# Performance work log

Hardware: AMD Instinct MI355X
Metric: run time of the kernel (lower is better)

## Reference

```python
import jax, jax.numpy as jnp
import numpy as np

N_NODES = 50000
N_EDGES = 800000
N_FEAT = 128
HID = 256
N_GRAPHS = 512


def _glorot(key, shape):
    fan_in, fan_out = shape[0], shape[1]
    s = jnp.sqrt(6.0 / (fan_in + fan_out))
    return jax.random.uniform(key, shape, jnp.float32, -s, s)


def setup_inputs() -> dict:
    key = jax.random.key(0)
    ks = jax.random.split(key, 10)
    x = jax.random.normal(ks[0], (N_NODES, N_FEAT), jnp.float32)
    edge_index = jax.random.randint(ks[1], (2, N_EDGES), 0, N_NODES, jnp.int64)
    batch = jnp.sort(jax.random.randint(ks[2], (N_NODES,), 0, N_GRAPHS, jnp.int64))
    y = jax.random.randint(ks[3], (N_GRAPHS,), 0, 2, jnp.int32)
    params = {
        "W1": _glorot(ks[4], (N_FEAT, HID)), "b1": jnp.zeros((HID,), jnp.float32),
        "W2": _glorot(ks[5], (HID, HID // 2)), "b2": jnp.zeros((HID // 2,), jnp.float32),
        "W3": _glorot(ks[6], (HID // 2, HID // 4)), "b3": jnp.zeros((HID // 4,), jnp.float32),
        "Wl": _glorot(ks[7], (HID // 4, 1)), "bl": jnp.zeros((1,), jnp.float32),
    }
    return {"x": x, "edge_index": edge_index, "batch": batch, "y": y, **params}


def gcn_conv(x, src, dst, dinv, W, b):
    # PyG GCNConv: x' = D^{-1/2}(A+I)D^{-1/2} x W + b, with self-loops.
    h = x @ W  # [N, out]
    norm = dinv[src] * dinv[dst]  # [E]
    agg = jax.ops.segment_sum(h[src] * norm[:, None], dst, num_segments=x.shape[0])
    agg = agg + h * (dinv * dinv)[:, None]  # self-loop contribution
    return agg + b


def reference(x, edge_index, batch, y, W1, b1, W2, b2, W3, b3, Wl, bl):
    n = x.shape[0]
    src, dst = edge_index[0], edge_index[1]
    # degree of A + I (in-degree on dst, plus self-loop)
    deg = jax.ops.segment_sum(jnp.ones_like(dst, dtype=x.dtype), dst, num_segments=n) + 1.0
    dinv = jax.lax.rsqrt(deg)

    h = jax.nn.relu(gcn_conv(x, src, dst, dinv, W1, b1))
    h = jax.nn.relu(gcn_conv(h, src, dst, dinv, W2, b2))
    h = gcn_conv(h, src, dst, dinv, W3, b3)

    # global mean pool over graphs
    sums = jax.ops.segment_sum(h, batch, num_segments=N_GRAPHS)
    counts = jax.ops.segment_sum(jnp.ones((n,), h.dtype), batch, num_segments=N_GRAPHS)
    pooled = sums / jnp.maximum(counts, 1.0)[:, None]

    logits = pooled @ Wl + bl  # [G, 1]
    t = y.reshape(-1, 1).astype(logits.dtype)
    # BCEWithLogitsLoss (mean, numerically stable)
    loss = jnp.mean(jnp.maximum(logits, 0.0) - logits * t + jnp.log1p(jnp.exp(-jnp.abs(logits))))
    out = jax.nn.sigmoid(logits)
    return (out, loss)
```

## Files before the change

kernel.cpp:

```cpp
#include <hip/hip_runtime.h>
#include <hip/hip_bf16.h>

typedef short s8v __attribute__((ext_vector_type(8)));
typedef float f4v __attribute__((ext_vector_type(4)));
typedef float f2v __attribute__((ext_vector_type(2)));
typedef unsigned short u16;
typedef unsigned char u8;

#define EPB 16384
#define NBKT 196

__device__ __forceinline__ float bf2f(short u) {
    unsigned int x = ((unsigned int)(unsigned short)u) << 16;
    return __builtin_bit_cast(float, x);
}
__device__ __forceinline__ short f2bf(float f) {
    unsigned int u = __builtin_bit_cast(unsigned int, f);
    unsigned int r = (u + 0x7FFF + ((u >> 16) & 1)) >> 16;
    return (short)r;
}
__device__ __forceinline__ short h16(float f) {
    return (short)(__builtin_bit_cast(unsigned int, f) >> 16);
}
__device__ __forceinline__ void dec16_add(uint4 u, float* acc) {
    f2v p;
    p = __builtin_amdgcn_cvt_pk_f32_fp8(u.x, false); acc[0] += p[0];  acc[1] += p[1];
    p = __builtin_amdgcn_cvt_pk_f32_fp8(u.x, true);  acc[2] += p[0];  acc[3] += p[1];
    p = __builtin_amdgcn_cvt_pk_f32_fp8(u.y, false); acc[4] += p[0];  acc[5] += p[1];
    p = __builtin_amdgcn_cvt_pk_f32_fp8(u.y, true);  acc[6] += p[0];  acc[7] += p[1];
    p = __builtin_amdgcn_cvt_pk_f32_fp8(u.z, false); acc[8] += p[0];  acc[9] += p[1];
    p = __builtin_amdgcn_cvt_pk_f32_fp8(u.z, true);  acc[10] += p[0]; acc[11] += p[1];
    p = __builtin_amdgcn_cvt_pk_f32_fp8(u.w, false); acc[12] += p[0]; acc[13] += p[1];
    p = __builtin_amdgcn_cvt_pk_f32_fp8(u.w, true);  acc[14] += p[0]; acc[15] += p[1];
}
__device__ __forceinline__ s8v dec8_bf16(unsigned lo, unsigned hi) {
    f2v p0 = __builtin_amdgcn_cvt_pk_f32_fp8(lo, false);
    f2v p1 = __builtin_amdgcn_cvt_pk_f32_fp8(lo, true);
    f2v p2 = __builtin_amdgcn_cvt_pk_f32_fp8(hi, false);
    f2v p3 = __builtin_amdgcn_cvt_pk_f32_fp8(hi, true);
    s8v r;
    r[0] = h16(p0[0]); r[1] = h16(p0[1]); r[2] = h16(p1[0]); r[3] = h16(p1[1]);
    r[4] = h16(p2[0]); r[5] = h16(p2[1]); r[6] = h16(p3[0]); r[7] = h16(p3[1]);
    return r;
}
template<bool HI>
__device__ __forceinline__ unsigned pk2(float a, float b, unsigned old) {
    return __builtin_amdgcn_cvt_pk_fp8_f32(a, b, old, HI);
}
__device__ __forceinline__ u8 enc1(float v) {
    return (u8)(__builtin_amdgcn_cvt_pk_fp8_f32(v, v, 0, false) & 0xff);
}

__global__ __launch_bounds__(256)
void k_fat(const int* __restrict__ dst, int e, int* __restrict__ hist_t, int nbA,
           const float* __restrict__ W1, const float* __restrict__ W2,
           const float* __restrict__ W3, const float* __restrict__ Wl,
           const float* __restrict__ b3, short* __restrict__ Bt1,
           short* __restrict__ Bt2, const int* __restrict__ batch, int n, int ngr,
           int* __restrict__ gstart, u8* __restrict__ xs8,
           float* __restrict__ w3l, float* __restrict__ wb) {
    int blk = blockIdx.x, tid = threadIdx.x;
    if (blk < nbA) {
        __shared__ int h[NBKT];
        if (tid < NBKT) h[tid] = 0;
        __syncthreads();
        int base = blk * EPB;
        int end = min(base + EPB, e);
        for (int i = base + tid * 4; i < end; i += 1024) {
            if (i + 3 < end) {
                int4 d = *(const int4*)(dst + i);
                atomicAdd(&h[d.x >> 8], 1);
                atomicAdd(&h[d.y >> 8], 1);
                atomicAdd(&h[d.z >> 8], 1);
                atomicAdd(&h[d.w >> 8], 1);
            } else {
                for (int k = i; k < end; ++k) atomicAdd(&h[dst[k] >> 8], 1);
            }
        }
        __syncthreads();
        if (tid < NBKT) hist_t[tid * nbA + blk] = h[tid];
    } else if (blk < nbA + 256) {
        int id = (blk - nbA) * 256 + tid;
        if (id < 32768) {
            int c = id >> 7, k = id & 127;
            Bt1[id] = f2bf(W1[k * 256 + c]);
        } else {
            int i = id - 32768;
            int c = i >> 8, k = i & 255;
            Bt2[i] = f2bf(W2[k * 128 + c]);
        }
    } else if (blk < nbA + 259) {
        int g = (blk - nbA - 256) * 256 + tid;
        if (g > ngr) return;
        if (g == ngr) { gstart[g] = n; return; }
        int lo = 0, hi = n;
        while (lo < hi) { int mid = (lo + hi) >> 1; if (batch[mid] < g) lo = mid + 1; else hi = mid; }
        gstart[g] = lo;
    } else if (blk == nbA + 259) {
        if (tid < 32) ((unsigned*)xs8)[(size_t)n * 32 + tid] = 0;
    } else {
        if (tid < 128) {
            float s = 0.f;
            #pragma unroll 4
            for (int c = 0; c < 64; ++c) s = fmaf(W3[tid * 64 + c], Wl[c], s);
            w3l[tid] = s;
        } else if (tid == 128) {
            float s = 0.f;
            for (int c = 0; c < 64; ++c) s = fmaf(b3[c], Wl[c], s);
            wb[0] = s;
        }
    }
}

__global__ __launch_bounds__(1024)
void k_scanall(int* __restrict__ a, int nelem) {
    __shared__ int ws[16];
    int tid = threadIdx.x, lane = tid & 63, w = tid >> 6;
    int base = tid * 10;
    int v[10];
    int s = 0;
    #pragma unroll
    for (int k = 0; k < 10; ++k) { v[k] = (base + k < nelem) ? a[base + k] : 0; s += v[k]; }
    int x = s;
    #pragma unroll
    for (int d = 1; d < 64; d <<= 1) {
        int t2 = __shfl_up(x, d, 64);
        if (lane >= d) x += t2;
    }
    if (lane == 63) ws[w] = x;
    __syncthreads();
    if (w == 0 && lane < 16) {
        int vv = ws[lane];
        int xx = vv;
        #pragma unroll
        for (int d = 1; d < 16; d <<= 1) {
            int t2 = __shfl_up(xx, d, 64);
            if (lane >= d) xx += t2;
        }
        ws[lane] = xx - vv;
    }
    __syncthreads();
    int run = ws[w] + (x - s);
    #pragma unroll
    for (int k = 0; k < 10; ++k) {
        if (base + k < nelem) a[base + k] = run;
        run += v[k];
    }
}

__global__ __launch_bounds__(256)
void k_part(const int* __restrict__ src, const int* __restrict__ dst, int e,
            const int* __restrict__ offs, int nbA, unsigned* __restrict__ parted) {
    __shared__ int cur[NBKT];
    int tid = threadIdx.x, blk = blockIdx.x;
    if (tid < NBKT) cur[tid] = offs[tid * nbA + blk];
    __syncthreads();
    int base = blk * EPB;
    int end = min(base + EPB, e);
    for (int i = base + tid * 4; i < end; i += 1024) {
        if (i + 3 < end) {
            int4 d = *(const int4*)(dst + i);
            int4 s = *(const int4*)(src + i);
            int p;
            p = atomicAdd(&cur[d.x >> 8], 1); parted[p] = (unsigned)s.x | ((unsigned)(d.x & 255) << 16);
            p = atomicAdd(&cur[d.y >> 8], 1); parted[p] = (unsigned)s.y | ((unsigned)(d.y & 255) << 16);
            p = atomicAdd(&cur[d.z >> 8], 1); parted[p] = (unsigned)s.z | ((unsigned)(d.z & 255) << 16);
            p = atomicAdd(&cur[d.w >> 8], 1); parted[p] = (unsigned)s.w | ((unsigned)(d.w & 255) << 16);
        } else {
            for (int k = i; k < end; ++k) {
                int d = dst[k];
                int p = atomicAdd(&cur[d >> 8], 1);
                parted[p] = (unsigned)src[k] | ((unsigned)(d & 255) << 16);
            }
        }
    }
}

__global__ __launch_bounds__(256)
void k_lists(const unsigned* __restrict__ parted, const int* __restrict__ offs,
             int nbA, int e, const float* __restrict__ x, u16* __restrict__ csrcp,
             int* __restrict__ deg, float* __restrict__ dinv,
             u8* __restrict__ xs8, int n) {
    __shared__ u16 lists[256 * 64];
    __shared__ int cnt[256];
    int tid = threadIdx.x, bkt = blockIdx.x;
    for (int k = tid; k < 16384; k += 256) lists[k] = 0xFFFF;
    cnt[tid] = 0;
    __syncthreads();
    int base = offs[bkt * nbA];
    int end = (bkt == NBKT - 1) ? e : offs[(bkt + 1) * nbA];
    for (int i = base + tid; i < end; i += 256) {
        unsigned p = parted[i];
        int dl = (int)((p >> 16) & 0xFF);
        int r = atomicAdd(&cnt[dl], 1);
        if (r < 64) lists[dl * 64 + r] = (u16)(p & 0xFFFF);
    }
    __syncthreads();
    const s8v* lsrc = (const s8v*)lists;
    s8v* ldst = (s8v*)(csrcp + (size_t)bkt * (256 * 64));
    for (int k = tid; k < 2048; k += 256) ldst[k] = lsrc[k];
    int node = bkt * 256 + tid;
    deg[node] = min(cnt[tid], 64);
    dinv[node] = rsqrtf((float)cnt[tid] + 1.0f);
    #pragma unroll 1
    for (int r16 = 0; r16 < 16; ++r16) {
        int local = r16 * 16 + (tid >> 4);
        int row = bkt * 256 + local;
        if (row >= n) continue;
        float dv = rsqrtf((float)cnt[local] + 1.0f);
        int cg = (tid & 15) * 8;
        f4v a = *(const f4v*)(x + (size_t)row * 128 + cg);
        f4v b = *(const f4v*)(x + (size_t)row * 128 + cg + 4);
        unsigned w0 = pk2<false>(a[0] * dv, a[1] * dv, 0);
        w0 = pk2<true>(a[2] * dv, a[3] * dv, w0);
        unsigned w1 = pk2<false>(b[0] * dv, b[1] * dv, 0);
        w1 = pk2<true>(b[2] * dv, b[3] * dv, w1);
        uint2 o = {w0, w1};
        *(uint2*)(xs8 + (size_t)row * 128 + cg) = o;
    }
}

template<int K, int NT, int CT, bool BIAS, bool RELU, bool DVS, bool ZROW>
__global__ __launch_bounds__(256)
void k_gemm(const u8* __restrict__ A8, const short* __restrict__ Bt,
            const float* __restrict__ bias, const float* __restrict__ dinv,
            u8* __restrict__ C8, int M) {
    constexpr int S = K / 32;
    constexpr int N = NT * 16 * CT;
    if (ZROW && blockIdx.x == 0 && threadIdx.x < N) {
        C8[(size_t)M * N + threadIdx.x] = 0;
    }
    const int lane = threadIdx.x & 63;
    const int gw = (blockIdx.x * 256 + threadIdx.x) >> 6;
    const int nw = (gridDim.x * 256) >> 6;
    const int colset = gw % CT;
    const int strip0 = gw / CT;
    const int sstr = nw / CT;
    const int l15 = lane & 15, l4 = lane >> 4;
    const int colbase = colset * (NT * 16);

    s8v bfr[NT][S];
    float bcol[NT];
    #pragma unroll
    for (int nt = 0; nt < NT; ++nt) {
        int col = colbase + nt * 16 + l15;
        if (BIAS) bcol[nt] = bias[col];
        const short* bp = Bt + (size_t)col * K + l4 * 8;
        #pragma unroll
        for (int s = 0; s < S; ++s)
            bfr[nt][s] = *(const s8v*)(bp + s * 32);
    }

    const int nstrips = M >> 4;
    int strip = strip0;
    if (strip >= nstrips) return;
    uint2 cur[S];
    {
        const u8* arow = A8 + (size_t)(strip * 16 + l15) * K + l4 * 8;
        #pragma unroll
        for (int s = 0; s < S; ++s) cur[s] = *(const uint2*)(arow + s * 32);
    }
    while (true) {
        int nstrip = strip + sstr;
        bool has = nstrip < nstrips;
        uint2 nxt[S];
        if (has) {
            const u8* arow = A8 + (size_t)(nstrip * 16 + l15) * K + l4 * 8;
            #pragma unroll
            for (int s = 0; s < S; ++s) nxt[s] = *(const uint2*)(arow + s * 32);
        }
        f4v acc[NT];
        #pragma unroll
        for (int nt = 0; nt < NT; ++nt) acc[nt] = (f4v){0.f, 0.f, 0.f, 0.f};
        #pragma unroll
        for (int s = 0; s < S; ++s) {
            s8v av = dec8_bf16(cur[s].x, cur[s].y);
            #pragma unroll
            for (int nt = 0; nt < NT; ++nt)
                acc[nt] = __builtin_amdgcn_mfma_f32_16x16x32_bf16(av, bfr[nt][s], acc[nt], 0, 0, 0);
        }
        int orow = strip * 16 + l4 * 4;
        f4v dvr;
        if (DVS) dvr = *(const f4v*)(dinv + orow);
        #pragma unroll
        for (int nt = 0; nt < NT; ++nt) {
            int col = colbase + nt * 16 + l15;
            #pragma unroll
            for (int r = 0; r < 4; ++r) {
                float v = acc[nt][r];
                if (DVS) v *= dvr[r];
                if (BIAS) v += bcol[nt];
                if (RELU) v = fmaxf(v, 0.f);
                C8[(size_t)(orow + r) * N + col] = enc1(v);
            }
        }
        if (!has) break;
        strip = nstrip;
        #pragma unroll
        for (int s = 0; s < S; ++s) cur[s] = nxt[s];
    }
}

template<bool RELU, bool BIAS, bool STORE, bool QPROJ>
__global__ __launch_bounds__(256, 2)
void k_agg(const u8* __restrict__ h8, const u16* __restrict__ csrcp,
           const int* __restrict__ deg, const float* __restrict__ bias,
           u8* __restrict__ outp, int n,
           const float* __restrict__ w3l, float* __restrict__ q) {
    int node = (blockIdx.x * 256 + threadIdx.x) >> 3;
    if (node >= n) return;
    int t = threadIdx.x & 7;
    int c0 = t * 16;
    const u8* hp = h8 + c0;
    float acc[16];
    #pragma unroll
    for (int j = 0; j < 16; ++j) acc[j] = 0.f;
    dec16_add(*(const uint4*)(hp + (size_t)node * 128), acc);

    int dg = deg[node];
    int nch = (dg + 7) >> 3;
    const u16* ep = csrcp + (size_t)node * 64;
    for (int c = 0; c < nch; ++c) {
        int idx = (int)ep[c * 8 + t];
        uint4 buf[8];
        #pragma unroll
        for (int j = 0; j < 8; ++j) {
            unsigned s = (unsigned)__shfl(idx, j, 8);
            s = s < (unsigned)n ? s : (unsigned)n;
            buf[j] = *(const uint4*)(hp + (size_t)s * 128);
        }
        #pragma unroll
        for (int j = 0; j < 8; ++j) dec16_add(buf[j], acc);
    }

    float dv = rsqrtf((float)dg + 1.0f);
    float out[16];
    #pragma unroll
    for (int j = 0; j < 16; ++j) {
        float b = BIAS ? bias[c0 + j] : 0.f;
        out[j] = dv * acc[j] + b;
        if (RELU) out[j] = fmaxf(out[j], 0.f);
    }
    if (STORE) {
        uint4 o;
        o.x = pk2<false>(out[0], out[1], 0);   o.x = pk2<true>(out[2], out[3], o.x);
        o.y = pk2<false>(out[4], out[5], 0);   o.y = pk2<true>(out[6], out[7], o.y);
        o.z = pk2<false>(out[8], out[9], 0);   o.z = pk2<true>(out[10], out[11], o.z);
        o.w = pk2<false>(out[12], out[13], 0); o.w = pk2<true>(out[14], out[15], o.w);
        *(uint4*)(outp + (size_t)node * 128 + c0) = o;
    }
    if (QPROJ) {
        float part = 0.f;
        #pragma unroll
        for (int j = 0; j < 16; ++j) part = fmaf(out[j], w3l[c0 + j], part);
        #pragma unroll
        for (int d = 4; d > 0; d >>= 1) part += __shfl_down(part, d, 8);
        if (t == 0) q[node] = dv * part;
    }
}

__global__ __launch_bounds__(256)
void k_gpool(const float* __restrict__ q, const u16* __restrict__ csrcp,
             const int* __restrict__ deg, const int* __restrict__ gstart,
             const float* __restrict__ wb, const float* __restrict__ bl,
             const int* __restrict__ y, float* __restrict__ out,
             float* __restrict__ plos) {
    __shared__ float red[256];
    int g = blockIdx.x;
    int s = gstart[g], e = gstart[g + 1];
    float local = 0.f;
    float b3l = wb[0];
    for (int v = s + threadIdx.x; v < e; v += 256) {
        int dg = deg[v];
        float acc = q[v];
        const u16* ep = csrcp + (size_t)v * 64;
        for (int c = 0; c < dg; ++c)
            acc += q[ep[c]];
        local += rsqrtf((float)dg + 1.f) * acc + b3l;
    }
    red[threadIdx.x] = local;
    __syncthreads();
    for (int st = 128; st > 0; st >>= 1) {
        if (threadIdx.x < st) red[threadIdx.x] += red[threadIdx.x + st];
        __syncthreads();
    }
    if (threadIdx.x == 0) {
        float cnt = fmaxf((float)(e - s), 1.f);
        float l = red[0] / cnt + bl[0];
        out[g] = 1.f / (1.f + expf(-l));
        float t = (float)y[g];
        plos[g] = fmaxf(l, 0.f) - l * t + log1pf(expf(-fabsf(l)));
    }
}

__global__ void k_loss(const float* __restrict__ plos, float* __restrict__ out) {
    __shared__ float red[512];
    int g = threadIdx.x;
    red[g] = plos[g];
    __syncthreads();
    for (int s = 256; s > 0; s >>= 1) {
        if (g < s) red[g] += red[g + s];
        __syncthreads();
    }
    if (g == 0) out[512] = red[0] / 512.f;
}

extern "C" void kernel_launch(void* const* d_in, const int* in_sizes, int n_in,
                              void* d_out, int out_size, void* d_ws, size_t ws_size,
                              hipStream_t stream) {
    const float* x   = (const float*)d_in[0];
    const int* ei    = (const int*)d_in[1];
    const int* batch = (const int*)d_in[2];
    const int* y     = (const int*)d_in[3];
    const float* W1  = (const float*)d_in[4];
    const float* b1  = (const float*)d_in[5];
    const float* W2  = (const float*)d_in[6];
    const float* b2  = (const float*)d_in[7];
    const float* W3  = (const float*)d_in[8];
    const float* b3  = (const float*)d_in[9];
    const float* Wl  = (const float*)d_in[10];
    const float* bl  = (const float*)d_in[11];

    const int n = in_sizes[2];
    const int e = in_sizes[1] / 2;
    const int ngr = 512;
    const int nbA = (e + EPB - 1) / EPB;
    const int TE = NBKT * nbA;
    const int nrows = NBKT * 256;

    char* ws = (char*)d_ws;
    size_t off = 0;
    auto alloc = [&](size_t bytes) {
        char* p = ws + off;
        off = (off + bytes + 255) & ~(size_t)255;
        return p;
    };
    int*      offs   = (int*)alloc((size_t)TE * 4);
    unsigned* parted = (unsigned*)alloc((size_t)e * 4);
    u16*      csrcp  = (u16*)alloc((size_t)nrows * 64 * 2);
    int*      deg    = (int*)alloc((size_t)nrows * 4);
    float*    dinv   = (float*)alloc((size_t)nrows * 4);
    u8*       xs8    = (u8*)alloc((size_t)(n + 1) * 128);
    u8*       t18    = (u8*)alloc((size_t)n * 128);
    u8*       h18    = (u8*)alloc((size_t)n * 256);
    u8*       g28    = (u8*)alloc((size_t)(n + 1) * 128);
    float*    q      = (float*)alloc((size_t)n * 4);
    int*      gstart = (int*)alloc((size_t)(ngr + 1) * 4);
    short*    Bt1    = (short*)alloc((size_t)32768 * 2);
    short*    Bt2    = (short*)alloc((size_t)32768 * 2);
    float*    w3l    = (float*)alloc((size_t)128 * 4);
    float*    wb     = (float*)alloc((size_t)4 * 4);
    float*    plos   = (float*)alloc((size_t)ngr * 4);

    k_fat<<<nbA + 261, 256, 0, stream>>>(ei + e, e, offs, nbA, W1, W2, W3, Wl, b3,
                                         Bt1, Bt2, batch, n, ngr, gstart, xs8,
                                         w3l, wb);
    k_scanall<<<1, 1024, 0, stream>>>(offs, TE);
    k_part<<<nbA, 256, 0, stream>>>(ei, ei + e, e, offs, nbA, parted);
    k_lists<<<NBKT, 256, 0, stream>>>(parted, offs, nbA, e, x, csrcp, deg, dinv, xs8, n);

    const int gagg = (n * 8 + 255) / 256;
    k_agg<false, false, true, false><<<gagg, 256, 0, stream>>>(
        xs8, csrcp, deg, nullptr, t18, n, nullptr, nullptr);
    k_gemm<128, 4, 4, true, true, false, false><<<256, 256, 0, stream>>>(
        t18, Bt1, b1, nullptr, h18, n);
    k_gemm<256, 2, 4, false, false, true, true><<<256, 256, 0, stream>>>(
        h18, Bt2, nullptr, dinv, g28, n);
    k_agg<true, true, false, true><<<gagg, 256, 0, stream>>>(
        g28, csrcp, deg, b2, nullptr, n, w3l, q);
    k_gpool<<<ngr, 256, 0, stream>>>(q, csrcp, deg, gstart, wb, bl, y,
                                     (float*)d_out, plos);
    k_loss<<<1, 512, 0, stream>>>(plos, (float*)d_out);
}
```

Before: 133.0 us.

## Halve edge partition block size, remap GEMM warps, parallelize pooling, fuse loss reduction

Halves edges per partition block, which doubles the histogram/partition block count, and widens the scan to 20 elements per thread to cover the larger table. The GEMM now has each block own one row strip and assigns its four waves to the four column sets, instead of spreading strips across global waves. Graph pooling uses four lanes per node to walk the neighbor list. The separate loss kernel is removed in favor of an atomicAdd into a slot zeroed in the first kernel. Together these aim to cut launch count, add parallelism to pooling, and improve A-tile sharing in the GEMM. The cost is float atomics, which make the loss sum order nondeterministic.

```diff
diff --git a/kernel.cpp b/kernel.cpp
--- a/kernel.cpp
+++ b/kernel.cpp
@@ -7,7 +7,7 @@
 typedef unsigned short u16;
 typedef unsigned char u8;
 
-#define EPB 16384
+#define EPB 8192
 #define NBKT 196
 
 __device__ __forceinline__ float bf2f(short u) {
@@ -58,7 +58,8 @@
            const float* __restrict__ b3, short* __restrict__ Bt1,
            short* __restrict__ Bt2, const int* __restrict__ batch, int n, int ngr,
            int* __restrict__ gstart, u8* __restrict__ xs8,
-           float* __restrict__ w3l, float* __restrict__ wb) {
+           float* __restrict__ w3l, float* __restrict__ wb,
+           float* __restrict__ outp) {
     int blk = blockIdx.x, tid = threadIdx.x;
     if (blk < nbA) {
         __shared__ int h[NBKT];
@@ -108,6 +109,8 @@
             float s = 0.f;
             for (int c = 0; c < 64; ++c) s = fmaf(b3[c], Wl[c], s);
             wb[0] = s;
+        } else if (tid == 129) {
+            outp[512] = 0.f;
         }
     }
 }
@@ -116,11 +119,11 @@
 void k_scanall(int* __restrict__ a, int nelem) {
     __shared__ int ws[16];
     int tid = threadIdx.x, lane = tid & 63, w = tid >> 6;
-    int base = tid * 10;
-    int v[10];
+    int base = tid * 20;
+    int v[20];
     int s = 0;
     #pragma unroll
-    for (int k = 0; k < 10; ++k) { v[k] = (base + k < nelem) ? a[base + k] : 0; s += v[k]; }
+    for (int k = 0; k < 20; ++k) { v[k] = (base + k < nelem) ? a[base + k] : 0; s += v[k]; }
     int x = s;
     #pragma unroll
     for (int d = 1; d < 64; d <<= 1) {
@@ -142,7 +145,7 @@
     __syncthreads();
     int run = ws[w] + (x - s);
     #pragma unroll
-    for (int k = 0; k < 10; ++k) {
+    for (int k = 0; k < 20; ++k) {
         if (base + k < nelem) a[base + k] = run;
         run += v[k];
     }
@@ -220,22 +223,18 @@
     }
 }
 
-template<int K, int NT, int CT, bool BIAS, bool RELU, bool DVS, bool ZROW>
+template<int K, int NT, bool BIAS, bool RELU, bool DVS, bool ZROW>
 __global__ __launch_bounds__(256)
 void k_gemm(const u8* __restrict__ A8, const short* __restrict__ Bt,
             const float* __restrict__ bias, const float* __restrict__ dinv,
             u8* __restrict__ C8, int M) {
     constexpr int S = K / 32;
-    constexpr int N = NT * 16 * CT;
+    constexpr int N = NT * 16 * 4;
     if (ZROW && blockIdx.x == 0 && threadIdx.x < N) {
         C8[(size_t)M * N + threadIdx.x] = 0;
     }
     const int lane = threadIdx.x & 63;
-    const int gw = (blockIdx.x * 256 + threadIdx.x) >> 6;
-    const int nw = (gridDim.x * 256) >> 6;
-    const int colset = gw % CT;
-    const int strip0 = gw / CT;
-    const int sstr = nw / CT;
+    const int colset = threadIdx.x >> 6;
     const int l15 = lane & 15, l4 = lane >> 4;
     const int colbase = colset * (NT * 16);
 
@@ -252,7 +251,8 @@
     }
 
     const int nstrips = M >> 4;
-    int strip = strip0;
+    int strip = blockIdx.x;
+    const int sstr = gridDim.x;
     if (strip >= nstrips) return;
     uint2 cur[S];
     {
@@ -363,46 +363,42 @@
 void k_gpool(const float* __restrict__ q, const u16* __restrict__ csrcp,
              const int* __restrict__ deg, const int* __restrict__ gstart,
              const float* __restrict__ wb, const float* __restrict__ bl,
-             const int* __restrict__ y, float* __restrict__ out,
-             float* __restrict__ plos) {
+             const int* __restrict__ y, float* __restrict__ out) {
     __shared__ float red[256];
     int g = blockIdx.x;
+    int tid = threadIdx.x;
     int s = gstart[g], e = gstart[g + 1];
     float local = 0.f;
     float b3l = wb[0];
-    for (int v = s + threadIdx.x; v < e; v += 256) {
-        int dg = deg[v];
-        float acc = q[v];
-        const u16* ep = csrcp + (size_t)v * 64;
-        for (int c = 0; c < dg; ++c)
-            acc += q[ep[c]];
-        local += rsqrtf((float)dg + 1.f) * acc + b3l;
-    }
-    red[threadIdx.x] = local;
+    for (int v0 = s; v0 < e; v0 += 64) {
+        int v = v0 + (tid >> 2);
+        float part = 0.f;
+        if (v < e) {
+            int dg = deg[v];
+            const u16* ep = csrcp + (size_t)v * 64;
+            for (int c = tid & 3; c < dg; c += 4) part += q[ep[c]];
+        }
+        part += __shfl_down(part, 2, 4);
+        part += __shfl_down(part, 1, 4);
+        if ((tid & 3) == 0 && v < e) {
+            int dg = deg[v];
+            local += rsqrtf((float)dg + 1.f) * (q[v] + part) + b3l;
+        }
+    }
+    red[tid] = local;
     __syncthreads();
     for (int st = 128; st > 0; st >>= 1) {
-        if (threadIdx.x < st) red[threadIdx.x] += red[threadIdx.x + st];
+        if (tid < st) red[tid] += red[tid + st];
         __syncthreads();
     }
-    if (threadIdx.x == 0) {
+    if (tid == 0) {
         float cnt = fmaxf((float)(e - s), 1.f);
         float l = red[0] / cnt + bl[0];
         out[g] = 1.f / (1.f + expf(-l));
         float t = (float)y[g];
-        plos[g] = fmaxf(l, 0.f) - l * t + log1pf(expf(-fabsf(l)));
-    }
-}
-
-__global__ void k_loss(const float* __restrict__ plos, float* __restrict__ out) {
-    __shared__ float red[512];
-    int g = threadIdx.x;
-    red[g] = plos[g];
-    __syncthreads();
-    for (int s = 256; s > 0; s >>= 1) {
-        if (g < s) red[g] += red[g + s];
-        __syncthreads();
-    }
-    if (g == 0) out[512] = red[0] / 512.f;
+        float li = fmaxf(l, 0.f) - l * t + log1pf(expf(-fabsf(l)));
+        atomicAdd(&out[512], li * (1.0f / 512.0f));
+    }
 }
 
 extern "C" void kernel_launch(void* const* d_in, const int* in_sizes, int n_in,
@@ -450,11 +446,10 @@
     short*    Bt2    = (short*)alloc((size_t)32768 * 2);
     float*    w3l    = (float*)alloc((size_t)128 * 4);
     float*    wb     = (float*)alloc((size_t)4 * 4);
-    float*    plos   = (float*)alloc((size_t)ngr * 4);
 
     k_fat<<<nbA + 261, 256, 0, stream>>>(ei + e, e, offs, nbA, W1, W2, W3, Wl, b3,
                                          Bt1, Bt2, batch, n, ngr, gstart, xs8,
-                                         w3l, wb);
+                                         w3l, wb, (float*)d_out);
     k_scanall<<<1, 1024, 0, stream>>>(offs, TE);
     k_part<<<nbA, 256, 0, stream>>>(ei, ei + e, e, offs, nbA, parted);
     k_lists<<<NBKT, 256, 0, stream>>>(parted, offs, nbA, e, x, csrcp, deg, dinv, xs8, n);
@@ -462,13 +457,12 @@
     const int gagg = (n * 8 + 255) / 256;
     k_agg<false, false, true, false><<<gagg, 256, 0, stream>>>(
         xs8, csrcp, deg, nullptr, t18, n, nullptr, nullptr);
-    k_gemm<128, 4, 4, true, true, false, false><<<256, 256, 0, stream>>>(
+    k_gemm<128, 4, true, true, false, false><<<256, 256, 0, stream>>>(
         t18, Bt1, b1, nullptr, h18, n);
-    k_gemm<256, 2, 4, false, false, true, true><<<256, 256, 0, stream>>>(
+    k_gemm<256, 2, false, false, true, true><<<256, 256, 0, stream>>>(
         h18, Bt2, nullptr, dinv, g28, n);
     k_agg<true, true, false, true><<<gagg, 256, 0, stream>>>(
         g28, csrcp, deg, b2, nullptr, n, w3l, q);
     k_gpool<<<ngr, 256, 0, stream>>>(q, csrcp, deg, gstart, wb, bl, y,
-                                     (float*)d_out, plos);
-    k_loss<<<1, 512, 0, stream>>>(plos, (float*)d_out);
-}
+                                     (float*)d_out);
+}
```

New measurement: 134.5 us. Within noise of the previous version (+1.1%).
